# Performance work log

Measured on AMD Instinct MI355X. Metric: run time of the kernel, lower is better.

The kernel has to match this reference:

```python
import jax, jax.numpy as jnp
from jax import lax
import numpy as np

B, L, V, E = 128, 1000, 20, 32
KS = (1, 3, 5, 9, 15, 21)
NF = 20          # filters per conv branch
H_ENC = 256      # bilstm hidden per direction
H_DEC = 512
N_STEPS = 10


def conv1d(x, w, b):
    # x: [B, Cin, L], w: [Cout, Cin, K]
    p = w.shape[-1] // 2
    y = lax.conv_general_dilated(x, w, (1,), [(p, p)],
                                 dimension_numbers=('NCH', 'OIH', 'NCH'))
    return y + b[None, :, None]


def lstm_scan(seq, w_ih, w_hh, b_ih, b_hh, hidden):
    # seq: [T, B, I]; PyTorch gate order i,f,g,o
    bsz = seq.shape[1]
    h0 = jnp.zeros((bsz, hidden), seq.dtype)
    c0 = jnp.zeros((bsz, hidden), seq.dtype)
    b = b_ih + b_hh

    def step(carry, xt):
        h, c = carry
        g = xt @ w_ih.T + h @ w_hh.T + b
        i, f, gg, o = jnp.split(g, 4, axis=-1)
        c = jax.nn.sigmoid(f) * c + jax.nn.sigmoid(i) * jnp.tanh(gg)
        h = jax.nn.sigmoid(o) * jnp.tanh(c)
        return (h, c), h

    _, hs = lax.scan(step, (h0, c0), seq)
    return hs  # [T, B, hidden]


def setup_inputs() -> dict:
    key = jax.random.key(0)
    keys = iter(jax.random.split(key, 64))

    def p(shape, s=0.05):
        return jax.random.normal(next(keys), shape, jnp.float32) * s

    inp = {"x": jax.random.randint(next(keys), (B, L), 0, V)}
    inp["embed_w"] = p((V, E), 0.5).at[0].set(0.0)  # padding_idx=0
    for i, k in enumerate(KS):
        inp[f"cw{i}"] = p((NF, E, k))
        inp[f"cb{i}"] = p((NF,))
    inp["conv2_w"] = p((128, 6 * NF, 3)); inp["conv2_b"] = p((128,))
    # bilstm forward / reverse
    inp["lstm_wif"] = p((4 * H_ENC, 128)); inp["lstm_whf"] = p((4 * H_ENC, H_ENC))
    inp["lstm_bif"] = p((4 * H_ENC,));    inp["lstm_bhf"] = p((4 * H_ENC,))
    inp["lstm_wir"] = p((4 * H_ENC, 128)); inp["lstm_whr"] = p((4 * H_ENC, H_ENC))
    inp["lstm_bir"] = p((4 * H_ENC,));    inp["lstm_bhr"] = p((4 * H_ENC,))
    # decoder LSTMCell (input 1024 -> hidden 512)
    inp["dec_wi"] = p((4 * H_DEC, 2 * H_DEC)); inp["dec_wh"] = p((4 * H_DEC, H_DEC))
    inp["dec_bi"] = p((4 * H_DEC,));           inp["dec_bh"] = p((4 * H_DEC,))
    # attention + heads
    inp["attn_v"] = p((256,), 1.0)
    inp["we_w"] = p((256, 512)); inp["we_b"] = p((256,))
    inp["wd_w"] = p((256, 512)); inp["wd_b"] = p((256,))
    inp["fc_w"] = p((512, 512)); inp["fc_b"] = p((512,))
    inp["out_w"] = p((8, 512));  inp["out_b"] = p((8,))
    inp["c0"] = p((512,), 1.0)
    return inp


def reference(x, embed_w, cw0, cb0, cw1, cb1, cw2, cb2, cw3, cb3, cw4, cb4,
              cw5, cb5, conv2_w, conv2_b,
              lstm_wif, lstm_whf, lstm_bif, lstm_bhf,
              lstm_wir, lstm_whr, lstm_bir, lstm_bhr,
              dec_wi, dec_wh, dec_bi, dec_bh,
              attn_v, we_w, we_b, wd_w, wd_b, fc_w, fc_b, out_w, out_b, c0):
    bsz = x.shape[0]
    h = embed_w[x]                      # [B, L, E]
    xc = h.transpose(0, 2, 1)           # [B, E, L]
    branches = [(cw0, cb0), (cw1, cb1), (cw2, cb2), (cw3, cb3), (cw4, cb4), (cw5, cb5)]
    cnn_cat = jnp.concatenate([jax.nn.relu(conv1d(xc, w, b)) for w, b in branches], axis=1)
    feat = jax.nn.relu(conv1d(cnn_cat, conv2_w, conv2_b))  # [B, 128, L]
    seq = feat.transpose(2, 0, 1)                          # [L, B, 128]
    hs_f = lstm_scan(seq, lstm_wif, lstm_whf, lstm_bif, lstm_bhf, H_ENC)
    hs_b = lstm_scan(seq[::-1], lstm_wir, lstm_whr, lstm_bir, lstm_bhr, H_ENC)[::-1]
    lstm_out = jnp.concatenate([hs_f, hs_b], axis=-1).transpose(1, 0, 2)  # [B, L, 512]

    # encoder projection is step-invariant: precompute W_e(lstm_out)
    e_enc = jnp.einsum('blh,eh->ble', lstm_out, we_w) + we_b  # [B, L, 256]
    dec_b = dec_bi + dec_bh

    def dec_step(carry, _):
        hd, cd, ctx = carry
        inp = jnp.concatenate([ctx, hd], axis=1)             # [B, 1024]
        g = inp @ dec_wi.T + hd @ dec_wh.T + dec_b
        i, f, gg, o = jnp.split(g, 4, axis=1)
        cd = jax.nn.sigmoid(f) * cd + jax.nn.sigmoid(i) * jnp.tanh(gg)
        hd = jax.nn.sigmoid(o) * jnp.tanh(cd)
        d = hd @ wd_w.T + wd_b                               # [B, 256]
        e = jnp.tanh(e_enc + d[:, None, :])                  # [B, L, 256]
        a = e @ attn_v                                       # [B, L]
        w = jax.nn.softmax(a, axis=1)
        ctx = jnp.einsum('bl,blh->bh', w, lstm_out)          # [B, 512]
        return (hd, cd, ctx), None

    h0 = jnp.zeros((bsz, H_DEC), lstm_out.dtype)
    c0s = jnp.zeros((bsz, H_DEC), lstm_out.dtype)
    ctx0 = jnp.broadcast_to(c0, (bsz, H_DEC))
    (_, _, ctx), _ = lax.scan(dec_step, (h0, c0s, ctx0), None, length=N_STEPS)

    z = jax.nn.relu(ctx @ fc_w.T + fc_b)
    return jax.nn.sigmoid(z @ out_w.T + out_b)               # [B, 8]
```

## Files before the change

### kernel.cpp

```cpp
#include <hip/hip_runtime.h>
#include <hip/hip_bf16.h>
#include <math.h>


typedef __bf16 bf16_t;
typedef __bf16 bf16x8 __attribute__((ext_vector_type(8)));
typedef float f32x4 __attribute__((ext_vector_type(4)));

__device__ __constant__ int KBS[6]  = {1, 3, 5, 9, 15, 21};
__device__ __constant__ int WOFF[6] = {0, 1024, 4096, 9216, 18432, 33792};

__device__ inline f32x4 mfma16(bf16x8 a, bf16x8 b, f32x4 c) {
  return __builtin_amdgcn_mfma_f32_16x16x32_bf16(a, b, c, 0, 0, 0);
}
__device__ inline float sigm(float x) { return 1.f / (1.f + __expf(-x)); }
__device__ inline float tanh_fast(float x) {
  x = fminf(15.f, fmaxf(-15.f, x));
  float e = __expf(2.f * x);
  return (e - 1.f) / (e + 1.f);
}

__device__ inline void store_h_ic(bf16_t* p, bf16_t v) {
  unsigned short b = __builtin_bit_cast(unsigned short, v);
  __hip_atomic_store((unsigned short*)p, b, __ATOMIC_RELAXED, __HIP_MEMORY_SCOPE_AGENT);
}

__global__ void k_init(bf16_t* H, unsigned* bar, bf16_t* feat1p, float* cd,
                       bf16_t* dec_in, float* cbias, const float* c0,
                       const float* cb0, const float* cb1, const float* cb2,
                       const float* cb3, const float* cb4, const float* cb5) {
  int i = blockIdx.x * 256 + threadIdx.x;
  if (i < 65536) {
    unsigned* Hu = (unsigned*)H;
    size_t off = (i < 32768) ? (size_t)i : ((size_t)1001 * 32768 + (i - 32768));
    __hip_atomic_store(Hu + off, 0u, __ATOMIC_RELAXED, __HIP_MEMORY_SCOPE_AGENT);
    return;
  }
  i -= 65536;
  if (i < 512) {
    __hip_atomic_store(bar + i, 0u, __ATOMIC_RELAXED, __HIP_MEMORY_SCOPE_AGENT);
    return;
  }
  i -= 512;
  if (i < 30720) {
    int b = i / 240; int r = i - b * 240;
    int row = (r < 120) ? 0 : 1001; int c = r % 120;
    feat1p[b * 120240 + row * 120 + c] = (bf16_t)0.f; return;
  }
  i -= 30720;
  if (i < 256) { feat1p[128 * 120240 + i] = (bf16_t)0.f; return; }
  i -= 256;
  if (i < 65536) { cd[i] = 0.f; return; }
  i -= 65536;
  if (i < 131072) { int k = i & 1023; dec_in[i] = (k < 512) ? (bf16_t)c0[k] : (bf16_t)0.f; return; }
  i -= 131072;
  if (i < 120) {
    const float* cbs[6] = {cb0, cb1, cb2, cb3, cb4, cb5};
    cbias[i] = cbs[i / 20][i % 20]; return;
  }
}

__global__ void k_prep_lstm(const float* wif, const float* whf, const float* bif, const float* bhf,
                            const float* wir, const float* whr, const float* bir, const float* bhr,
                            bf16_t* Wl, float* bl) {
  int row = blockIdx.x;
  int dir = row >> 10; int np = row & 1023;
  int tile = np >> 6; int rem = np & 63; int g = rem >> 4; int u = rem & 15;
  int orow = g * 256 + tile * 16 + u;
  const float* wi = dir ? wir : wif;
  const float* wh = dir ? whr : whf;
  for (int k = threadIdx.x; k < 384; k += blockDim.x) {
    float v = (k < 128) ? wi[orow * 128 + k] : wh[orow * 256 + (k - 128)];
    Wl[row * 384 + k] = (bf16_t)v;
  }
  if (threadIdx.x == 0) {
    const float* bi = dir ? bir : bif;
    const float* bh = dir ? bhr : bhf;
    bl[row] = bi[orow] + bh[orow];
  }
}

__global__ void k_prep_dec(const float* dwi, const float* dwh, const float* dbi, const float* dbh,
                           bf16_t* Wdec, float* bdec) {
  int np = blockIdx.x;
  int tile = np >> 6; int rem = np & 63; int g = rem >> 4; int u = rem & 15;
  int orow = g * 512 + tile * 16 + u;
  for (int k = threadIdx.x; k < 1024; k += blockDim.x) {
    float v;
    if (k < 512) v = dwi[orow * 1024 + k];
    else v = dwi[orow * 1024 + 512 + (k - 512)] + dwh[orow * 512 + (k - 512)];
    Wdec[np * 1024 + k] = (bf16_t)v;
  }
  if (threadIdx.x == 0) bdec[np] = dbi[orow] + dbh[orow];
}

__global__ void k_prep_misc(const float* cw0, const float* cw1, const float* cw2,
                            const float* cw3, const float* cw4, const float* cw5,
                            const float* conv2_w, const float* we_w, const float* wd_w,
                            bf16_t* Wc1, bf16_t* Wc2, bf16_t* Wwe, bf16_t* Wwd) {
  int i = blockIdx.x * 256 + threadIdx.x;
  if (i < 55296) {
    const float* cws[6] = {cw0, cw1, cw2, cw3, cw4, cw5};
    int br = 0;
    while (br < 5 && i >= WOFF[br + 1]) ++br;
    int K = KBS[br];
    int jj = i - WOFF[br];
    int kw = K * 32;
    int f = jj / kw; int rem = jj - f * kw; int k = rem >> 5; int c = rem & 31;
    float v = (f < 20) ? cws[br][(f * 32 + c) * K + k] : 0.f;
    Wc1[i] = (bf16_t)v;
    return;
  }
  i -= 55296;
  if (i < 49152) {
    int co = i / 384; int kk = i - co * 384;
    float v = 0.f;
    if (kk < 360) { int ci = kk % 120; int k = kk / 120; v = conv2_w[co * 360 + ci * 3 + k]; }
    Wc2[i] = (bf16_t)v;
    return;
  }
  i -= 49152;
  if (i < 131072) { Wwe[i] = (bf16_t)we_w[i]; return; }
  i -= 131072;
  if (i < 131072) { Wwd[i] = (bf16_t)wd_w[i]; return; }
}

__global__ void k_embed(const int* x, const float* ew, bf16_t* embp) {
  int idx = blockIdx.x * 256 + threadIdx.x;
  if (idx >= 128 * 1020 * 32) return;
  int c = idx & 31; int rest = idx >> 5;
  int j = rest % 1020; int b = rest / 1020;
  float v = 0.f;
  int l = j - 10;
  if (l >= 0 && l < 1000) { int tok = x[b * 1000 + l]; v = ew[tok * 32 + c]; }
  embp[idx] = (bf16_t)v;
}

__global__ void __launch_bounds__(256) k_conv1(const bf16_t* __restrict__ embp,
                                               const bf16_t* __restrict__ Wc1,
                                               const float* __restrict__ cbias,
                                               bf16_t* __restrict__ feat1p) {
  int tile = blockIdx.x, br = blockIdx.y;
  int Kb = KBS[br]; int p = Kb >> 1;
  const bf16_t* Wb = Wc1 + WOFF[br];
  int tid = threadIdx.x; int w = tid >> 6; int lane = tid & 63; int u = lane & 15; int q = lane >> 4;
  const bf16_t* arow[2];
#pragma unroll
  for (int mf = 0; mf < 2; ++mf) {
    int r = tile * 128 + w * 32 + mf * 16 + u;
    int b = r / 1000, l = r - b * 1000;
    arow[mf] = embp + b * 32640 + (l + 10 - p) * 32;
  }
  f32x4 acc[2][2];
#pragma unroll
  for (int mf = 0; mf < 2; ++mf)
#pragma unroll
    for (int nf = 0; nf < 2; ++nf) acc[mf][nf] = (f32x4){0.f, 0.f, 0.f, 0.f};
  int kw = Kb * 32;
  for (int kc = 0; kc < Kb; ++kc) {
    int kk = kc * 32 + q * 8;
    bf16x8 a0 = *(const bf16x8*)(arow[0] + kk);
    bf16x8 a1 = *(const bf16x8*)(arow[1] + kk);
    bf16x8 b0 = *(const bf16x8*)(Wb + u * kw + kk);
    bf16x8 b1 = *(const bf16x8*)(Wb + (16 + u) * kw + kk);
    acc[0][0] = mfma16(a0, b0, acc[0][0]);
    acc[0][1] = mfma16(a0, b1, acc[0][1]);
    acc[1][0] = mfma16(a1, b0, acc[1][0]);
    acc[1][1] = mfma16(a1, b1, acc[1][1]);
  }
#pragma unroll
  for (int nf = 0; nf < 2; ++nf) {
    int n = nf * 16 + u;
    if (n >= 20) continue;
    int fg = br * 20 + n;
    float bias = cbias[fg];
#pragma unroll
    for (int mf = 0; mf < 2; ++mf)
#pragma unroll
      for (int reg = 0; reg < 4; ++reg) {
        int r = tile * 128 + w * 32 + mf * 16 + q * 4 + reg;
        int b = r / 1000, l = r - b * 1000;
        float v = acc[mf][nf][reg] + bias;
        v = fmaxf(v, 0.f);
        feat1p[b * 120240 + (l + 1) * 120 + fg] = (bf16_t)v;
      }
  }
}

__global__ void __launch_bounds__(256) k_conv2(const bf16_t* __restrict__ feat1p,
                                               const bf16_t* __restrict__ Wc2,
                                               const float* __restrict__ c2b,
                                               bf16_t* __restrict__ seq) {
  int tile = blockIdx.x;
  int tid = threadIdx.x; int w = tid >> 6; int lane = tid & 63; int u = lane & 15; int q = lane >> 4;
  const bf16_t* arow[2];
#pragma unroll
  for (int mf = 0; mf < 2; ++mf) {
    int r = tile * 128 + w * 32 + mf * 16 + u;
    int b = r / 1000, l = r - b * 1000;
    arow[mf] = feat1p + b * 120240 + l * 120;
  }
  f32x4 acc[2][8];
#pragma unroll
  for (int mf = 0; mf < 2; ++mf)
#pragma unroll
    for (int nf = 0; nf < 8; ++nf) acc[mf][nf] = (f32x4){0.f, 0.f, 0.f, 0.f};
#pragma unroll
  for (int kc = 0; kc < 12; ++kc) {
    int kk = kc * 32 + q * 8;
    bf16x8 a0 = *(const bf16x8*)(arow[0] + kk);
    bf16x8 a1 = *(const bf16x8*)(arow[1] + kk);
#pragma unroll
    for (int nf = 0; nf < 8; ++nf) {
      bf16x8 bfr = *(const bf16x8*)(Wc2 + (nf * 16 + u) * 384 + kk);
      acc[0][nf] = mfma16(a0, bfr, acc[0][nf]);
      acc[1][nf] = mfma16(a1, bfr, acc[1][nf]);
    }
  }
#pragma unroll
  for (int nf = 0; nf < 8; ++nf) {
    int n = nf * 16 + u;
    float bias = c2b[n];
#pragma unroll
    for (int mf = 0; mf < 2; ++mf)
#pragma unroll
      for (int reg = 0; reg < 4; ++reg) {
        int r = tile * 128 + w * 32 + mf * 16 + q * 4 + reg;
        int b = r / 1000, l = r - b * 1000;
        float v = fmaxf(acc[mf][nf][reg] + bias, 0.f);
        seq[(l * 128 + b) * 128 + n] = (bf16_t)v;
      }
  }
}

__global__ void __launch_bounds__(256) k_lstm(const bf16_t* __restrict__ seq,
                                              const bf16_t* __restrict__ Wl,
                                              const float* __restrict__ bl,
                                              bf16_t* H, unsigned* bar) {
  const int bid = blockIdx.x;
  const int dir = bid >> 4;
  const int tile = bid & 15;
  const int tid = threadIdx.x;
  const int w = tid >> 6, lane = tid & 63, u = lane & 15, q = lane >> 4;

  __shared__ __align__(16) bf16_t Wlds[64 * 392];
  const bf16_t* Wg = Wl + (size_t)(dir * 1024 + tile * 64) * 384;
  for (int i = tid; i < 64 * 48; i += 256) {
    int rr = i / 48, cc = (i - rr * 48) * 8;
    *(bf16x8*)&Wlds[rr * 392 + cc] = *(const bf16x8*)&Wg[rr * 384 + cc];
  }
  float bias[4];
#pragma unroll
  for (int g = 0; g < 4; ++g) bias[g] = bl[dir * 1024 + tile * 64 + g * 16 + u];
  __syncthreads();

  const int j = tile * 16 + u;
  const int mA0 = w * 32 + u, mA1 = w * 32 + 16 + u;
  float creg[2][4] = {{0.f, 0.f, 0.f, 0.f}, {0.f, 0.f, 0.f, 0.f}};
  unsigned* flg = bar + dir * 256;

  bf16x8 pf[2][4];
  {
    const bf16_t* seqt = seq + (size_t)(dir ? 999 : 0) * 16384;
#pragma unroll
    for (int kc = 0; kc < 4; ++kc) {
      pf[0][kc] = *(const bf16x8*)&seqt[mA0 * 128 + kc * 32 + q * 8];
      pf[1][kc] = *(const bf16x8*)&seqt[mA1 * 128 + kc * 32 + q * 8];
    }
  }

  for (int s = 0; s < 1000; ++s) {
    int t = dir ? (999 - s) : s;
    const bf16_t* hread = H + ((size_t)(dir ? (t + 2) : t) * 2 + dir) * 32768;
    bf16_t* hwrite = H + ((size_t)(t + 1) * 2 + dir) * 32768;

    bf16x8 hv0[8], hv1[8];
#pragma unroll
    for (int i = 0; i < 8; ++i) {
      hv0[i] = *(const bf16x8*)&hread[mA0 * 256 + i * 32 + q * 8];
      hv1[i] = *(const bf16x8*)&hread[mA1 * 256 + i * 32 + q * 8];
    }

    f32x4 acc[2][4];
#pragma unroll
    for (int mf = 0; mf < 2; ++mf)
#pragma unroll
      for (int g = 0; g < 4; ++g) acc[mf][g] = (f32x4){0.f, 0.f, 0.f, 0.f};

#pragma unroll
    for (int kc = 0; kc < 4; ++kc) {
      int kk = kc * 32 + q * 8;
#pragma unroll
      for (int g = 0; g < 4; ++g) {
        bf16x8 bfr = *(const bf16x8*)&Wlds[(g * 16 + u) * 392 + kk];
        acc[0][g] = mfma16(pf[0][kc], bfr, acc[0][g]);
        acc[1][g] = mfma16(pf[1][kc], bfr, acc[1][g]);
      }
    }
#pragma unroll
    for (int i = 0; i < 8; ++i) {
      int kk = 128 + i * 32 + q * 8;
#pragma unroll
      for (int g = 0; g < 4; ++g) {
        bf16x8 bfr = *(const bf16x8*)&Wlds[(g * 16 + u) * 392 + kk];
        acc[0][g] = mfma16(hv0[i], bfr, acc[0][g]);
        acc[1][g] = mfma16(hv1[i], bfr, acc[1][g]);
      }
    }

    if (s < 999) {
      const bf16_t* seqn = seq + (size_t)(dir ? (t - 1) : (t + 1)) * 16384;
#pragma unroll
      for (int kc = 0; kc < 4; ++kc) {
        pf[0][kc] = *(const bf16x8*)&seqn[mA0 * 128 + kc * 32 + q * 8];
        pf[1][kc] = *(const bf16x8*)&seqn[mA1 * 128 + kc * 32 + q * 8];
      }
    }

#pragma unroll
    for (int mf = 0; mf < 2; ++mf) {
#pragma unroll
      for (int reg = 0; reg < 4; ++reg) {
        int m = w * 32 + mf * 16 + q * 4 + reg;
        float gi = sigm(acc[mf][0][reg] + bias[0]);
        float gf = sigm(acc[mf][1][reg] + bias[1]);
        float gg = tanh_fast(acc[mf][2][reg] + bias[2]);
        float go = sigm(acc[mf][3][reg] + bias[3]);
        float c = gf * creg[mf][reg] + gi * gg;
        creg[mf][reg] = c;
        store_h_ic(&hwrite[m * 256 + j], (bf16_t)(go * tanh_fast(c)));
      }
    }

    if (s < 999) {
      __syncthreads();
      if (tid == 0)
        __hip_atomic_store(&flg[tile * 16], (unsigned)(s + 1), __ATOMIC_RELAXED,
                           __HIP_MEMORY_SCOPE_AGENT);
      if (w == 0) {
        unsigned target = (unsigned)(s + 1);
        int spins = 0;
        while (spins < (1 << 17)) {
          unsigned f = (lane < 16)
              ? __hip_atomic_load(&flg[lane * 16], __ATOMIC_RELAXED, __HIP_MEMORY_SCOPE_AGENT)
              : target;
          if (__ballot(f >= target) == ~0ull) break;
          __builtin_amdgcn_s_sleep(1);
          ++spins;
        }
      }
      __syncthreads();
    }
  }
}

__global__ void __launch_bounds__(256) k_eenc(const bf16_t* __restrict__ H,
                                              const bf16_t* __restrict__ Wwe,
                                              const float* __restrict__ we_b,
                                              bf16_t* __restrict__ e_enc) {
  int mt = blockIdx.x;
  int n0 = blockIdx.y * 64;
  int tid = threadIdx.x; int w = tid >> 6; int lane = tid & 63; int u = lane & 15; int q = lane >> 4;
  const bf16_t* af[2]; const bf16_t* ar[2];
#pragma unroll
  for (int mf = 0; mf < 2; ++mf) {
    int b = w * 32 + mf * 16 + u;
    af[mf] = H + (((size_t)(mt + 1) * 2 + 0) * 128 + b) * 256;
    ar[mf] = H + (((size_t)(mt + 1) * 2 + 1) * 128 + b) * 256;
  }
  f32x4 acc[2][4];
#pragma unroll
  for (int mf = 0; mf < 2; ++mf)
#pragma unroll
    for (int nf = 0; nf < 4; ++nf) acc[mf][nf] = (f32x4){0.f, 0.f, 0.f, 0.f};
#pragma unroll
  for (int kc = 0; kc < 16; ++kc) {
    int kk = (kc & 7) * 32 + q * 8;
    bf16x8 a0 = (kc < 8) ? *(const bf16x8*)(af[0] + kk) : *(const bf16x8*)(ar[0] + kk);
    bf16x8 a1 = (kc < 8) ? *(const bf16x8*)(af[1] + kk) : *(const bf16x8*)(ar[1] + kk);
#pragma unroll
    for (int nf = 0; nf < 4; ++nf) {
      bf16x8 bfr = *(const bf16x8*)(Wwe + (n0 + nf * 16 + u) * 512 + kc * 32 + q * 8);
      acc[0][nf] = mfma16(a0, bfr, acc[0][nf]);
      acc[1][nf] = mfma16(a1, bfr, acc[1][nf]);
    }
  }
#pragma unroll
  for (int nf = 0; nf < 4; ++nf) {
    int n = n0 + nf * 16 + u;
    float bias = we_b[n];
#pragma unroll
    for (int mf = 0; mf < 2; ++mf)
#pragma unroll
      for (int reg = 0; reg < 4; ++reg) {
        int r = mt * 128 + w * 32 + mf * 16 + q * 4 + reg;
        e_enc[(size_t)n * 128000 + r] = (bf16_t)(acc[mf][nf][reg] + bias);
      }
  }
}

__global__ void __launch_bounds__(256) k_dec_gates(const bf16_t* __restrict__ dec_in,
                                                   const bf16_t* __restrict__ Wdec,
                                                   const float* __restrict__ bdec,
                                                   float* __restrict__ cd,
                                                   bf16_t* __restrict__ hd_new) {
  int tile = blockIdx.x;
  int tid = threadIdx.x; int w = tid >> 6; int lane = tid & 63; int u = lane & 15; int q = lane >> 4;
  int j = tile * 16 + u;
  float bias[4];
#pragma unroll
  for (int g = 0; g < 4; ++g) bias[g] = bdec[tile * 64 + g * 16 + u];
  int mA0 = w * 32 + u, mA1 = w * 32 + 16 + u;
  f32x4 acc[2][4];
#pragma unroll
  for (int mf = 0; mf < 2; ++mf)
#pragma unroll
    for (int g = 0; g < 4; ++g) acc[mf][g] = (f32x4){0.f, 0.f, 0.f, 0.f};
#pragma unroll 4
  for (int kc = 0; kc < 32; ++kc) {
    int kk = kc * 32 + q * 8;
    bf16x8 a0 = *(const bf16x8*)&dec_in[mA0 * 1024 + kk];
    bf16x8 a1 = *(const bf16x8*)&dec_in[mA1 * 1024 + kk];
#pragma unroll
    for (int g = 0; g < 4; ++g) {
      bf16x8 bfr = *(const bf16x8*)&Wdec[(size_t)(tile * 64 + g * 16 + u) * 1024 + kk];
      acc[0][g] = mfma16(a0, bfr, acc[0][g]);
      acc[1][g] = mfma16(a1, bfr, acc[1][g]);
    }
  }
#pragma unroll
  for (int mf = 0; mf < 2; ++mf) {
#pragma unroll
    for (int reg = 0; reg < 4; ++reg) {
      int m = w * 32 + mf * 16 + q * 4 + reg;
      float gi = sigm(acc[mf][0][reg] + bias[0]);
      float gf = sigm(acc[mf][1][reg] + bias[1]);
      float gg = tanh_fast(acc[mf][2][reg] + bias[2]);
      float go = sigm(acc[mf][3][reg] + bias[3]);
      float c = gf * cd[m * 512 + j] + gi * gg;
      cd[m * 512 + j] = c;
      hd_new[m * 512 + j] = (bf16_t)(go * tanh_fast(c));
    }
  }
}

__global__ void __launch_bounds__(256) k_d(const bf16_t* __restrict__ hd_new,
                                           const bf16_t* __restrict__ Wwd,
                                           const float* __restrict__ wd_b,
                                           float* __restrict__ d_t) {
  int n0 = blockIdx.x * 64;
  int tid = threadIdx.x; int w = tid >> 6; int lane = tid & 63; int u = lane & 15; int q = lane >> 4;
  int mA0 = w * 32 + u, mA1 = w * 32 + 16 + u;
  f32x4 acc[2][4];
#pragma unroll
  for (int mf = 0; mf < 2; ++mf)
#pragma unroll
    for (int nf = 0; nf < 4; ++nf) acc[mf][nf] = (f32x4){0.f, 0.f, 0.f, 0.f};
#pragma unroll
  for (int kc = 0; kc < 16; ++kc) {
    int kk = kc * 32 + q * 8;
    bf16x8 a0 = *(const bf16x8*)&hd_new[mA0 * 512 + kk];
    bf16x8 a1 = *(const bf16x8*)&hd_new[mA1 * 512 + kk];
#pragma unroll
    for (int nf = 0; nf < 4; ++nf) {
      bf16x8 bfr = *(const bf16x8*)&Wwd[(n0 + nf * 16 + u) * 512 + kk];
      acc[0][nf] = mfma16(a0, bfr, acc[0][nf]);
      acc[1][nf] = mfma16(a1, bfr, acc[1][nf]);
    }
  }
#pragma unroll
  for (int nf = 0; nf < 4; ++nf) {
    int n = n0 + nf * 16 + u;
    float bias = wd_b[n];
#pragma unroll
    for (int mf = 0; mf < 2; ++mf)
#pragma unroll
      for (int reg = 0; reg < 4; ++reg) {
        int m = w * 32 + mf * 16 + q * 4 + reg;
        d_t[n * 128 + m] = acc[mf][nf][reg] + bias;
      }
  }
}

__global__ void __launch_bounds__(256) k_score(const bf16_t* __restrict__ e_enc,
                                               const float* __restrict__ d_t,
                                               const float* __restrict__ attn_v,
                                               float* __restrict__ scores) {
  int tid = threadIdx.x;
  __shared__ float vl[256];
  vl[tid] = attn_v[tid];
  __syncthreads();
  int sub = tid >> 7, b = tid & 127;
  int l = blockIdx.x * 2 + sub;
  const bf16_t* ep = e_enc + (size_t)l * 128 + b;
  const float* dp = d_t + b;
  float acc = 0.f;
#pragma unroll 8
  for (int n = 0; n < 256; ++n)
    acc += tanh_fast((float)ep[(size_t)n * 128000] + dp[n * 128]) * vl[n];
  scores[b * 1000 + l] = acc;
}

__global__ void __launch_bounds__(512) k_softmax_ctx(const float* __restrict__ scores,
                                                     const bf16_t* __restrict__ H,
                                                     const bf16_t* __restrict__ hd_new,
                                                     bf16_t* __restrict__ dec_in) {
  int b = blockIdx.x;
  int tid = threadIdx.x; int wid = tid >> 6; int lane = tid & 63;
  __shared__ float wls[1000];
  __shared__ float red[8];
  __shared__ float sh_scalar;
  float mx = -1e30f;
  for (int l = tid; l < 1000; l += 512) {
    float s = scores[b * 1000 + l];
    wls[l] = s;
    mx = fmaxf(mx, s);
  }
#pragma unroll
  for (int off = 32; off > 0; off >>= 1) mx = fmaxf(mx, __shfl_xor(mx, off));
  if (lane == 0) red[wid] = mx;
  __syncthreads();
  if (tid == 0) {
    float m2 = red[0];
#pragma unroll
    for (int i = 1; i < 8; ++i) m2 = fmaxf(m2, red[i]);
    sh_scalar = m2;
  }
  __syncthreads();
  mx = sh_scalar;
  float sum = 0.f;
  for (int l = tid; l < 1000; l += 512) {
    float p = __expf(wls[l] - mx);
    wls[l] = p;
    sum += p;
  }
#pragma unroll
  for (int off = 32; off > 0; off >>= 1) sum += __shfl_xor(sum, off);
  if (lane == 0) red[wid] = sum;
  __syncthreads();
  if (tid == 0) {
    float s2 = red[0];
#pragma unroll
    for (int i = 1; i < 8; ++i) s2 += red[i];
    sh_scalar = s2;
  }
  __syncthreads();
  float inv = 1.f / sh_scalar;
  int dirr = tid >> 8, hh = tid & 255;
  float acc = 0.f;
  const bf16_t* lp = H + (size_t)65536 + (size_t)dirr * 32768 + b * 256 + hh;
#pragma unroll 4
  for (int l = 0; l < 1000; ++l) acc += wls[l] * (float)lp[(size_t)l * 65536];
  dec_in[b * 1024 + tid] = (bf16_t)(acc * inv);
  dec_in[b * 1024 + 512 + tid] = hd_new[b * 512 + tid];
}

__global__ void __launch_bounds__(256) k_fc_out(const bf16_t* __restrict__ dec_in,
                                                const float* __restrict__ fc_w,
                                                const float* __restrict__ fc_b,
                                                const float* __restrict__ out_w,
                                                const float* __restrict__ out_b,
                                                float* __restrict__ out) {
  int b = blockIdx.x;
  int tid = threadIdx.x;
  __shared__ float ctxs[512], zs[512], parts[32][8];
  for (int jj = tid; jj < 512; jj += 256) ctxs[jj] = (float)dec_in[b * 1024 + jj];
  __syncthreads();
  for (int n = tid; n < 512; n += 256) {
    float acc = fc_b[n];
    const float* wr = fc_w + n * 512;
    for (int k = 0; k < 512; ++k) acc += ctxs[k] * wr[k];
    zs[n] = fmaxf(acc, 0.f);
  }
  __syncthreads();
  int col = tid & 7, part = tid >> 3;
  float acc = 0.f;
  const float* wo = out_w + col * 512;
  for (int k = part * 16; k < part * 16 + 16; ++k) acc += zs[k] * wo[k];
  parts[part][col] = acc;
  __syncthreads();
  if (tid < 8) {
    float a = out_b[tid];
    for (int p2 = 0; p2 < 32; ++p2) a += parts[p2][tid];
    out[b * 8 + tid] = 1.f / (1.f + __expf(-a));
  }
}

extern "C" void kernel_launch(void* const* d_in, const int* in_sizes, int n_in,
                              void* d_out, int out_size, void* d_ws, size_t ws_size,
                              hipStream_t stream) {
  const int*   x       = (const int*)d_in[0];
  const float* embed_w = (const float*)d_in[1];
  const float* cw[6]   = {(const float*)d_in[2], (const float*)d_in[4], (const float*)d_in[6],
                          (const float*)d_in[8], (const float*)d_in[10], (const float*)d_in[12]};
  const float* cb[6]   = {(const float*)d_in[3], (const float*)d_in[5], (const float*)d_in[7],
                          (const float*)d_in[9], (const float*)d_in[11], (const float*)d_in[13]};
  const float* conv2_w = (const float*)d_in[14];
  const float* conv2_b = (const float*)d_in[15];
  const float* lstm_wif = (const float*)d_in[16];
  const float* lstm_whf = (const float*)d_in[17];
  const float* lstm_bif = (const float*)d_in[18];
  const float* lstm_bhf = (const float*)d_in[19];
  const float* lstm_wir = (const float*)d_in[20];
  const float* lstm_whr = (const float*)d_in[21];
  const float* lstm_bir = (const float*)d_in[22];
  const float* lstm_bhr = (const float*)d_in[23];
  const float* dec_wi  = (const float*)d_in[24];
  const float* dec_wh  = (const float*)d_in[25];
  const float* dec_bi  = (const float*)d_in[26];
  const float* dec_bh  = (const float*)d_in[27];
  const float* attn_v  = (const float*)d_in[28];
  const float* we_w    = (const float*)d_in[29];
  const float* we_b    = (const float*)d_in[30];
  const float* wd_w    = (const float*)d_in[31];
  const float* wd_b    = (const float*)d_in[32];
  const float* fc_w    = (const float*)d_in[33];
  const float* fc_b    = (const float*)d_in[34];
  const float* out_w   = (const float*)d_in[35];
  const float* out_b   = (const float*)d_in[36];
  const float* c0      = (const float*)d_in[37];
  float* out = (float*)d_out;

  char* base = (char*)d_ws;
  bf16_t* feat1p  = (bf16_t*)(base + 0);
  bf16_t* seq     = (bf16_t*)(base + 30781952);
  bf16_t* embp    = (bf16_t*)(base + 63549952);
  bf16_t* e_enc   = (bf16_t*)(base + 0);
  char* p = base + 71905792;
  auto alloc = [&](size_t bytes) { char* r = p; p += (bytes + 255) & ~(size_t)255; return r; };
  bf16_t* H       = (bf16_t*)alloc((size_t)1002 * 65536 * 2);
  bf16_t* Wl      = (bf16_t*)alloc((size_t)2 * 1024 * 384 * 2);
  float*  bl      = (float*)alloc(2048 * 4);
  bf16_t* Wc1     = (bf16_t*)alloc(55296 * 2);
  float*  cbias   = (float*)alloc(512);
  bf16_t* Wc2     = (bf16_t*)alloc(49152 * 2);
  bf16_t* Wdec    = (bf16_t*)alloc((size_t)2048 * 1024 * 2);
  float*  bdec    = (float*)alloc(2048 * 4);
  bf16_t* Wwe     = (bf16_t*)alloc(131072 * 2);
  bf16_t* Wwd     = (bf16_t*)alloc(131072 * 2);
  unsigned* bar   = (unsigned*)alloc(512 * 4);
  bf16_t* dec_in  = (bf16_t*)alloc(131072 * 2);
  bf16_t* hd_new  = (bf16_t*)alloc(65536 * 2);
  float*  cd      = (float*)alloc(65536 * 4);
  float*  d_t     = (float*)alloc(32768 * 4);
  float*  scores  = (float*)alloc(128000 * 4);
  (void)ws_size; (void)n_in; (void)in_sizes; (void)out_size;

  k_init<<<1148, 256, 0, stream>>>(H, bar, feat1p, cd, dec_in, cbias, c0,
                                   cb[0], cb[1], cb[2], cb[3], cb[4], cb[5]);
  k_prep_lstm<<<2048, 128, 0, stream>>>(lstm_wif, lstm_whf, lstm_bif, lstm_bhf,
                                        lstm_wir, lstm_whr, lstm_bir, lstm_bhr, Wl, bl);
  k_prep_dec<<<2048, 256, 0, stream>>>(dec_wi, dec_wh, dec_bi, dec_bh, Wdec, bdec);
  k_prep_misc<<<1432, 256, 0, stream>>>(cw[0], cw[1], cw[2], cw[3], cw[4], cw[5],
                                        conv2_w, we_w, wd_w, Wc1, Wc2, Wwe, Wwd);
  k_embed<<<16320, 256, 0, stream>>>(x, embed_w, embp);
  k_conv1<<<dim3(1000, 6), 256, 0, stream>>>(embp, Wc1, cbias, feat1p);
  k_conv2<<<1000, 256, 0, stream>>>(feat1p, Wc2, conv2_b, seq);
  k_lstm<<<32, 256, 0, stream>>>(seq, Wl, bl, H, bar);
  k_eenc<<<dim3(1000, 4), 256, 0, stream>>>(H, Wwe, we_b, e_enc);
  for (int step = 0; step < 10; ++step) {
    k_dec_gates<<<32, 256, 0, stream>>>(dec_in, Wdec, bdec, cd, hd_new);
    k_d<<<4, 256, 0, stream>>>(hd_new, Wwd, wd_b, d_t);
    k_score<<<500, 256, 0, stream>>>(e_enc, d_t, attn_v, scores);
    k_softmax_ctx<<<128, 512, 0, stream>>>(scores, H, hd_new, dec_in);
  }
  k_fc_out<<<128, 256, 0, stream>>>(dec_in, fc_w, fc_b, out_w, out_b, out);
}
```

Baseline: 7.066 ms.

## Replace LSTM flag barrier with tagged h ring buffer; split context reduction

The bidirectional LSTM no longer uses a per-step flag barrier with __syncthreads and spin loops. Each h value is now written into a 4-deep ring buffer as a 32-bit word that carries the step number in its upper half. Consumers poll their own h slice until every tag matches, so each block waits only for its own data instead of on a global barrier. Separately, the attention context sum is split over 4 sequence chunks with atomicAdd into an fp32 buffer, plus a pack kernel, to raise decoder parallelism. The ring doubles the bytes per h read, and the atomics make the float sum order nondeterministic.

Result: slower. 15.02 ms (+112.6%).

```diff
diff --git a/kernel.cpp b/kernel.cpp
--- a/kernel.cpp
+++ b/kernel.cpp
@@ -6,6 +6,7 @@
 typedef __bf16 bf16_t;
 typedef __bf16 bf16x8 __attribute__((ext_vector_type(8)));
 typedef float f32x4 __attribute__((ext_vector_type(4)));
+typedef unsigned long long u64;
 
 __device__ __constant__ int KBS[6]  = {1, 3, 5, 9, 15, 21};
 __device__ __constant__ int WOFF[6] = {0, 1024, 4096, 9216, 18432, 33792};
@@ -20,28 +21,18 @@
   return (e - 1.f) / (e + 1.f);
 }
 
-__device__ inline void store_h_ic(bf16_t* p, bf16_t v) {
-  unsigned short b = __builtin_bit_cast(unsigned short, v);
-  __hip_atomic_store((unsigned short*)p, b, __ATOMIC_RELAXED, __HIP_MEMORY_SCOPE_AGENT);
-}
-
-__global__ void k_init(bf16_t* H, unsigned* bar, bf16_t* feat1p, float* cd,
-                       bf16_t* dec_in, float* cbias, const float* c0,
+__device__ inline void store_ic(unsigned* p, unsigned v) {
+  __hip_atomic_store(p, v, __ATOMIC_RELAXED, __HIP_MEMORY_SCOPE_AGENT);
+}
+__device__ inline u64 load_ic8(const u64* p) {
+  return __hip_atomic_load(p, __ATOMIC_RELAXED, __HIP_MEMORY_SCOPE_AGENT);
+}
+
+__global__ void k_init(bf16_t* feat1p, float* cd, bf16_t* dec_in, float* cbias,
+                       const float* c0,
                        const float* cb0, const float* cb1, const float* cb2,
                        const float* cb3, const float* cb4, const float* cb5) {
   int i = blockIdx.x * 256 + threadIdx.x;
-  if (i < 65536) {
-    unsigned* Hu = (unsigned*)H;
-    size_t off = (i < 32768) ? (size_t)i : ((size_t)1001 * 32768 + (i - 32768));
-    __hip_atomic_store(Hu + off, 0u, __ATOMIC_RELAXED, __HIP_MEMORY_SCOPE_AGENT);
-    return;
-  }
-  i -= 65536;
-  if (i < 512) {
-    __hip_atomic_store(bar + i, 0u, __ATOMIC_RELAXED, __HIP_MEMORY_SCOPE_AGENT);
-    return;
-  }
-  i -= 512;
   if (i < 30720) {
     int b = i / 240; int r = i - b * 240;
     int row = (r < 120) ? 0 : 1001; int c = r % 120;
@@ -233,10 +224,10 @@
   }
 }
 
-__global__ void __launch_bounds__(256) k_lstm(const bf16_t* __restrict__ seq,
-                                              const bf16_t* __restrict__ Wl,
-                                              const float* __restrict__ bl,
-                                              bf16_t* H, unsigned* bar) {
+__global__ void __launch_bounds__(256, 1) k_lstm(const bf16_t* __restrict__ seq,
+                                                 const bf16_t* __restrict__ Wl,
+                                                 const float* __restrict__ bl,
+                                                 bf16_t* H, unsigned* hx) {
   const int bid = blockIdx.x;
   const int dir = bid >> 4;
   const int tile = bid & 15;
@@ -257,7 +248,7 @@
   const int j = tile * 16 + u;
   const int mA0 = w * 32 + u, mA1 = w * 32 + 16 + u;
   float creg[2][4] = {{0.f, 0.f, 0.f, 0.f}, {0.f, 0.f, 0.f, 0.f}};
-  unsigned* flg = bar + dir * 256;
+  unsigned* ring = hx + dir * 32768;
 
   bf16x8 pf[2][4];
   {
@@ -271,14 +262,21 @@
 
   for (int s = 0; s < 1000; ++s) {
     int t = dir ? (999 - s) : s;
-    const bf16_t* hread = H + ((size_t)(dir ? (t + 2) : t) * 2 + dir) * 32768;
     bf16_t* hwrite = H + ((size_t)(t + 1) * 2 + dir) * 32768;
 
-    bf16x8 hv0[8], hv1[8];
-#pragma unroll
-    for (int i = 0; i < 8; ++i) {
-      hv0[i] = *(const bf16x8*)&hread[mA0 * 256 + i * 32 + q * 8];
-      hv1[i] = *(const bf16x8*)&hread[mA1 * 256 + i * 32 + q * 8];
+    u64 dv0[32], dv1[32];
+    const u64* a0 = nullptr; const u64* a1 = nullptr;
+    if (s > 0) {
+      const u64* rb = (const u64*)(hx + ((unsigned)(s - 1) & 3u) * 65536 + dir * 32768);
+      a0 = rb + mA0 * 128 + q * 4;
+      a1 = rb + mA1 * 128 + q * 4;
+#pragma unroll
+      for (int i = 0; i < 8; ++i)
+#pragma unroll
+        for (int pp = 0; pp < 4; ++pp) {
+          dv0[i * 4 + pp] = load_ic8(a0 + i * 16 + pp);
+          dv1[i * 4 + pp] = load_ic8(a1 + i * 16 + pp);
+        }
     }
 
     f32x4 acc[2][4];
@@ -297,14 +295,47 @@
         acc[1][g] = mfma16(pf[1][kc], bfr, acc[1][g]);
       }
     }
-#pragma unroll
-    for (int i = 0; i < 8; ++i) {
-      int kk = 128 + i * 32 + q * 8;
-#pragma unroll
-      for (int g = 0; g < 4; ++g) {
-        bf16x8 bfr = *(const bf16x8*)&Wlds[(g * 16 + u) * 392 + kk];
-        acc[0][g] = mfma16(hv0[i], bfr, acc[0][g]);
-        acc[1][g] = mfma16(hv1[i], bfr, acc[1][g]);
+
+    if (s > 0) {
+      unsigned tg = (unsigned)s;
+      int guard = 0;
+      for (;;) {
+        unsigned bad = 0;
+#pragma unroll
+        for (int i2 = 0; i2 < 32; ++i2) {
+          unsigned lo0 = (unsigned)dv0[i2], hi0 = (unsigned)(dv0[i2] >> 32);
+          unsigned lo1 = (unsigned)dv1[i2], hi1 = (unsigned)(dv1[i2] >> 32);
+          bad |= (lo0 >> 16) ^ tg;
+          bad |= (hi0 >> 16) ^ tg;
+          bad |= (lo1 >> 16) ^ tg;
+          bad |= (hi1 >> 16) ^ tg;
+        }
+        if (bad == 0 || ++guard > (1 << 17)) break;
+#pragma unroll
+        for (int i = 0; i < 8; ++i)
+#pragma unroll
+          for (int pp = 0; pp < 4; ++pp) {
+            dv0[i * 4 + pp] = load_ic8(a0 + i * 16 + pp);
+            dv1[i * 4 + pp] = load_ic8(a1 + i * 16 + pp);
+          }
+      }
+#pragma unroll
+      for (int i = 0; i < 8; ++i) {
+        union { unsigned u4[4]; bf16x8 v; } h0, h1;
+#pragma unroll
+        for (int pp = 0; pp < 4; ++pp) {
+          h0.u4[pp] = __builtin_amdgcn_perm((unsigned)(dv0[i * 4 + pp] >> 32),
+                                            (unsigned)dv0[i * 4 + pp], 0x05040100);
+          h1.u4[pp] = __builtin_amdgcn_perm((unsigned)(dv1[i * 4 + pp] >> 32),
+                                            (unsigned)dv1[i * 4 + pp], 0x05040100);
+        }
+        int kk = 128 + i * 32 + q * 8;
+#pragma unroll
+        for (int g = 0; g < 4; ++g) {
+          bf16x8 bfr = *(const bf16x8*)&Wlds[(g * 16 + u) * 392 + kk];
+          acc[0][g] = mfma16(h0.v, bfr, acc[0][g]);
+          acc[1][g] = mfma16(h1.v, bfr, acc[1][g]);
+        }
       }
     }
 
@@ -317,6 +348,8 @@
       }
     }
 
+    unsigned* rw = ring + ((unsigned)s & 3u) * 65536;
+    unsigned tagw = ((unsigned)(s + 1)) << 16;
 #pragma unroll
     for (int mf = 0; mf < 2; ++mf) {
 #pragma unroll
@@ -328,28 +361,11 @@
         float go = sigm(acc[mf][3][reg] + bias[3]);
         float c = gf * creg[mf][reg] + gi * gg;
         creg[mf][reg] = c;
-        store_h_ic(&hwrite[m * 256 + j], (bf16_t)(go * tanh_fast(c)));
-      }
-    }
-
-    if (s < 999) {
-      __syncthreads();
-      if (tid == 0)
-        __hip_atomic_store(&flg[tile * 16], (unsigned)(s + 1), __ATOMIC_RELAXED,
-                           __HIP_MEMORY_SCOPE_AGENT);
-      if (w == 0) {
-        unsigned target = (unsigned)(s + 1);
-        int spins = 0;
-        while (spins < (1 << 17)) {
-          unsigned f = (lane < 16)
-              ? __hip_atomic_load(&flg[lane * 16], __ATOMIC_RELAXED, __HIP_MEMORY_SCOPE_AGENT)
-              : target;
-          if (__ballot(f >= target) == ~0ull) break;
-          __builtin_amdgcn_s_sleep(1);
-          ++spins;
-        }
-      }
-      __syncthreads();
+        bf16_t hv = (bf16_t)(go * tanh_fast(c));
+        hwrite[m * 256 + j] = hv;
+        unsigned hb = (unsigned)__builtin_bit_cast(unsigned short, hv);
+        store_ic(&rw[m * 256 + j], tagw | hb);
+      }
     }
   }
 }
@@ -447,9 +463,12 @@
 __global__ void __launch_bounds__(256) k_d(const bf16_t* __restrict__ hd_new,
                                            const bf16_t* __restrict__ Wwd,
                                            const float* __restrict__ wd_b,
-                                           float* __restrict__ d_t) {
+                                           float* __restrict__ d_t,
+                                           float* __restrict__ ctxf) {
   int n0 = blockIdx.x * 64;
   int tid = threadIdx.x; int w = tid >> 6; int lane = tid & 63; int u = lane & 15; int q = lane >> 4;
+  int gz = blockIdx.x * 256 + tid;
+  for (int z = gz; z < 65536; z += 1024) ctxf[z] = 0.f;
   int mA0 = w * 32 + u, mA1 = w * 32 + 16 + u;
   f32x4 acc[2][4];
 #pragma unroll
@@ -501,11 +520,10 @@
   scores[b * 1000 + l] = acc;
 }
 
-__global__ void __launch_bounds__(512) k_softmax_ctx(const float* __restrict__ scores,
-                                                     const bf16_t* __restrict__ H,
-                                                     const bf16_t* __restrict__ hd_new,
-                                                     bf16_t* __restrict__ dec_in) {
-  int b = blockIdx.x;
+__global__ void __launch_bounds__(512) k_ctx(const float* __restrict__ scores,
+                                             const bf16_t* __restrict__ H,
+                                             float* __restrict__ ctxf) {
+  int chunk = blockIdx.x, b = blockIdx.y;
   int tid = threadIdx.x; int wid = tid >> 6; int lane = tid & 63;
   __shared__ float wls[1000];
   __shared__ float red[8];
@@ -548,10 +566,18 @@
   float inv = 1.f / sh_scalar;
   int dirr = tid >> 8, hh = tid & 255;
   float acc = 0.f;
-  const bf16_t* lp = H + (size_t)65536 + (size_t)dirr * 32768 + b * 256 + hh;
+  const bf16_t* lp = H + (size_t)65536 + (size_t)dirr * 32768 + b * 256 + hh +
+                     (size_t)(chunk * 250) * 65536;
 #pragma unroll 4
-  for (int l = 0; l < 1000; ++l) acc += wls[l] * (float)lp[(size_t)l * 65536];
-  dec_in[b * 1024 + tid] = (bf16_t)(acc * inv);
+  for (int l = 0; l < 250; ++l) acc += wls[chunk * 250 + l] * (float)lp[(size_t)l * 65536];
+  atomicAdd(&ctxf[b * 512 + tid], acc * inv);
+}
+
+__global__ void __launch_bounds__(512) k_pack(const float* __restrict__ ctxf,
+                                              const bf16_t* __restrict__ hd_new,
+                                              bf16_t* __restrict__ dec_in) {
+  int b = blockIdx.x; int tid = threadIdx.x;
+  dec_in[b * 1024 + tid] = (bf16_t)ctxf[b * 512 + tid];
   dec_in[b * 1024 + 512 + tid] = hd_new[b * 512 + tid];
 }
 
@@ -629,6 +655,7 @@
   char* p = base + 71905792;
   auto alloc = [&](size_t bytes) { char* r = p; p += (bytes + 255) & ~(size_t)255; return r; };
   bf16_t* H       = (bf16_t*)alloc((size_t)1002 * 65536 * 2);
+  unsigned* hx    = (unsigned*)alloc((size_t)4 * 2 * 128 * 256 * 4);
   bf16_t* Wl      = (bf16_t*)alloc((size_t)2 * 1024 * 384 * 2);
   float*  bl      = (float*)alloc(2048 * 4);
   bf16_t* Wc1     = (bf16_t*)alloc(55296 * 2);
@@ -638,16 +665,16 @@
   float*  bdec    = (float*)alloc(2048 * 4);
   bf16_t* Wwe     = (bf16_t*)alloc(131072 * 2);
   bf16_t* Wwd     = (bf16_t*)alloc(131072 * 2);
-  unsigned* bar   = (unsigned*)alloc(512 * 4);
   bf16_t* dec_in  = (bf16_t*)alloc(131072 * 2);
   bf16_t* hd_new  = (bf16_t*)alloc(65536 * 2);
   float*  cd      = (float*)alloc(65536 * 4);
   float*  d_t     = (float*)alloc(32768 * 4);
+  float*  ctxf    = (float*)alloc(65536 * 4);
   float*  scores  = (float*)alloc(128000 * 4);
   (void)ws_size; (void)n_in; (void)in_sizes; (void)out_size;
 
-  k_init<<<1148, 256, 0, stream>>>(H, bar, feat1p, cd, dec_in, cbias, c0,
-                                   cb[0], cb[1], cb[2], cb[3], cb[4], cb[5]);
+  k_init<<<890, 256, 0, stream>>>(feat1p, cd, dec_in, cbias, c0,
+                                  cb[0], cb[1], cb[2], cb[3], cb[4], cb[5]);
   k_prep_lstm<<<2048, 128, 0, stream>>>(lstm_wif, lstm_whf, lstm_bif, lstm_bhf,
                                         lstm_wir, lstm_whr, lstm_bir, lstm_bhr, Wl, bl);
   k_prep_dec<<<2048, 256, 0, stream>>>(dec_wi, dec_wh, dec_bi, dec_bh, Wdec, bdec);
@@ -656,13 +683,14 @@
   k_embed<<<16320, 256, 0, stream>>>(x, embed_w, embp);
   k_conv1<<<dim3(1000, 6), 256, 0, stream>>>(embp, Wc1, cbias, feat1p);
   k_conv2<<<1000, 256, 0, stream>>>(feat1p, Wc2, conv2_b, seq);
-  k_lstm<<<32, 256, 0, stream>>>(seq, Wl, bl, H, bar);
+  k_lstm<<<32, 256, 0, stream>>>(seq, Wl, bl, H, hx);
   k_eenc<<<dim3(1000, 4), 256, 0, stream>>>(H, Wwe, we_b, e_enc);
   for (int step = 0; step < 10; ++step) {
     k_dec_gates<<<32, 256, 0, stream>>>(dec_in, Wdec, bdec, cd, hd_new);
-    k_d<<<4, 256, 0, stream>>>(hd_new, Wwd, wd_b, d_t);
+    k_d<<<4, 256, 0, stream>>>(hd_new, Wwd, wd_b, d_t, ctxf);
     k_score<<<500, 256, 0, stream>>>(e_enc, d_t, attn_v, scores);
-    k_softmax_ctx<<<128, 512, 0, stream>>>(scores, H, hd_new, dec_in);
+    k_ctx<<<dim3(4, 128), 512, 0, stream>>>(scores, H, ctxf);
+    k_pack<<<128, 512, 0, stream>>>(ctxf, hd_new, dec_in);
   }
   k_fc_out<<<128, 256, 0, stream>>>(dec_in, fc_w, fc_b, out_w, out_b, out);
 }
```

## Use per-wave flags in LSTM recurrence and split decoder context over sequence chunks

Applied to the files above, without the earlier changes.

Replaces the block-wide __syncthreads barrier in the LSTM recurrence with per-wave flags. Each wave publishes its progress and polls only the matching waves of the other tiles. The input projection MFMAs are issued before the wait so they overlap the poll latency. It also splits the attention context reduction into four sequence chunks per batch, combined with atomicAdd into an fp32 buffer that k_d zeroes, plus a separate pack kernel. The cost is one extra launch per decoder step, non-deterministic float summation order, and subtle memory-ordering risk, since waves rely on relaxed atomics and vmcnt waits rather than block barriers.

After: 7.240 ms. 2.5% more time.

```diff
diff --git a/kernel.cpp b/kernel.cpp
--- a/kernel.cpp
+++ b/kernel.cpp
@@ -6,6 +6,7 @@
 typedef __bf16 bf16_t;
 typedef __bf16 bf16x8 __attribute__((ext_vector_type(8)));
 typedef float f32x4 __attribute__((ext_vector_type(4)));
+typedef unsigned long long u64;
 
 __device__ __constant__ int KBS[6]  = {1, 3, 5, 9, 15, 21};
 __device__ __constant__ int WOFF[6] = {0, 1024, 4096, 9216, 18432, 33792};
@@ -20,28 +21,24 @@
   return (e - 1.f) / (e + 1.f);
 }
 
+__device__ inline void store_ic(unsigned* p, unsigned v) {
+  __hip_atomic_store(p, v, __ATOMIC_RELAXED, __HIP_MEMORY_SCOPE_AGENT);
+}
+__device__ inline unsigned load_ic(const unsigned* p) {
+  return __hip_atomic_load(p, __ATOMIC_RELAXED, __HIP_MEMORY_SCOPE_AGENT);
+}
 __device__ inline void store_h_ic(bf16_t* p, bf16_t v) {
   unsigned short b = __builtin_bit_cast(unsigned short, v);
   __hip_atomic_store((unsigned short*)p, b, __ATOMIC_RELAXED, __HIP_MEMORY_SCOPE_AGENT);
 }
 
-__global__ void k_init(bf16_t* H, unsigned* bar, bf16_t* feat1p, float* cd,
-                       bf16_t* dec_in, float* cbias, const float* c0,
+__global__ void k_init(unsigned* bar, bf16_t* feat1p, float* cd, bf16_t* dec_in,
+                       float* cbias, const float* c0,
                        const float* cb0, const float* cb1, const float* cb2,
                        const float* cb3, const float* cb4, const float* cb5) {
   int i = blockIdx.x * 256 + threadIdx.x;
-  if (i < 65536) {
-    unsigned* Hu = (unsigned*)H;
-    size_t off = (i < 32768) ? (size_t)i : ((size_t)1001 * 32768 + (i - 32768));
-    __hip_atomic_store(Hu + off, 0u, __ATOMIC_RELAXED, __HIP_MEMORY_SCOPE_AGENT);
-    return;
-  }
-  i -= 65536;
-  if (i < 512) {
-    __hip_atomic_store(bar + i, 0u, __ATOMIC_RELAXED, __HIP_MEMORY_SCOPE_AGENT);
-    return;
-  }
-  i -= 512;
+  if (i < 2048) { store_ic(bar + i, 0u); return; }
+  i -= 2048;
   if (i < 30720) {
     int b = i / 240; int r = i - b * 240;
     int row = (r < 120) ? 0 : 1001; int c = r % 120;
@@ -233,10 +230,10 @@
   }
 }
 
-__global__ void __launch_bounds__(256) k_lstm(const bf16_t* __restrict__ seq,
-                                              const bf16_t* __restrict__ Wl,
-                                              const float* __restrict__ bl,
-                                              bf16_t* H, unsigned* bar) {
+__global__ void __launch_bounds__(256, 1) k_lstm(const bf16_t* __restrict__ seq,
+                                                 const bf16_t* __restrict__ Wl,
+                                                 const float* __restrict__ bl,
+                                                 bf16_t* H, unsigned* bar) {
   const int bid = blockIdx.x;
   const int dir = bid >> 4;
   const int tile = bid & 15;
@@ -257,7 +254,8 @@
   const int j = tile * 16 + u;
   const int mA0 = w * 32 + u, mA1 = w * 32 + 16 + u;
   float creg[2][4] = {{0.f, 0.f, 0.f, 0.f}, {0.f, 0.f, 0.f, 0.f}};
-  unsigned* flg = bar + dir * 256;
+  unsigned* myflag = bar + ((dir * 16 + tile) * 4 + w) * 16;
+  const unsigned* pollp = bar + ((dir * 16 + (lane & 15)) * 4 + w) * 16;
 
   bf16x8 pf[2][4];
   {
@@ -271,15 +269,12 @@
 
   for (int s = 0; s < 1000; ++s) {
     int t = dir ? (999 - s) : s;
+    bf16_t* hwrite = H + ((size_t)(t + 1) * 2 + dir) * 32768;
     const bf16_t* hread = H + ((size_t)(dir ? (t + 2) : t) * 2 + dir) * 32768;
-    bf16_t* hwrite = H + ((size_t)(t + 1) * 2 + dir) * 32768;
-
-    bf16x8 hv0[8], hv1[8];
-#pragma unroll
-    for (int i = 0; i < 8; ++i) {
-      hv0[i] = *(const bf16x8*)&hread[mA0 * 256 + i * 32 + q * 8];
-      hv1[i] = *(const bf16x8*)&hread[mA1 * 256 + i * 32 + q * 8];
-    }
+
+    unsigned tgt = (unsigned)s;
+    unsigned f0 = tgt;
+    if (s > 0 && lane < 16) f0 = load_ic(pollp);
 
     f32x4 acc[2][4];
 #pragma unroll
@@ -297,14 +292,29 @@
         acc[1][g] = mfma16(pf[1][kc], bfr, acc[1][g]);
       }
     }
-#pragma unroll
-    for (int i = 0; i < 8; ++i) {
-      int kk = 128 + i * 32 + q * 8;
-#pragma unroll
-      for (int g = 0; g < 4; ++g) {
-        bf16x8 bfr = *(const bf16x8*)&Wlds[(g * 16 + u) * 392 + kk];
-        acc[0][g] = mfma16(hv0[i], bfr, acc[0][g]);
-        acc[1][g] = mfma16(hv1[i], bfr, acc[1][g]);
+
+    if (s > 0) {
+      unsigned f = f0;
+      int guard = 0;
+      while (__ballot(f >= tgt) != ~0ull && guard < (1 << 20)) {
+        f = (lane < 16) ? load_ic(pollp) : tgt;
+        ++guard;
+      }
+      bf16x8 hv0[8], hv1[8];
+#pragma unroll
+      for (int i = 0; i < 8; ++i) {
+        hv0[i] = *(const bf16x8*)&hread[mA0 * 256 + i * 32 + q * 8];
+        hv1[i] = *(const bf16x8*)&hread[mA1 * 256 + i * 32 + q * 8];
+      }
+#pragma unroll
+      for (int i = 0; i < 8; ++i) {
+        int kk = 128 + i * 32 + q * 8;
+#pragma unroll
+        for (int g = 0; g < 4; ++g) {
+          bf16x8 bfr = *(const bf16x8*)&Wlds[(g * 16 + u) * 392 + kk];
+          acc[0][g] = mfma16(hv0[i], bfr, acc[0][g]);
+          acc[1][g] = mfma16(hv1[i], bfr, acc[1][g]);
+        }
       }
     }
 
@@ -332,25 +342,8 @@
       }
     }
 
-    if (s < 999) {
-      __syncthreads();
-      if (tid == 0)
-        __hip_atomic_store(&flg[tile * 16], (unsigned)(s + 1), __ATOMIC_RELAXED,
-                           __HIP_MEMORY_SCOPE_AGENT);
-      if (w == 0) {
-        unsigned target = (unsigned)(s + 1);
-        int spins = 0;
-        while (spins < (1 << 17)) {
-          unsigned f = (lane < 16)
-              ? __hip_atomic_load(&flg[lane * 16], __ATOMIC_RELAXED, __HIP_MEMORY_SCOPE_AGENT)
-              : target;
-          if (__ballot(f >= target) == ~0ull) break;
-          __builtin_amdgcn_s_sleep(1);
-          ++spins;
-        }
-      }
-      __syncthreads();
-    }
+    asm volatile("s_waitcnt vmcnt(0)" ::: "memory");
+    if (lane == 0) store_ic(myflag, (unsigned)(s + 1));
   }
 }
 
@@ -447,9 +440,12 @@
 __global__ void __launch_bounds__(256) k_d(const bf16_t* __restrict__ hd_new,
                                            const bf16_t* __restrict__ Wwd,
                                            const float* __restrict__ wd_b,
-                                           float* __restrict__ d_t) {
+                                           float* __restrict__ d_t,
+                                           float* __restrict__ ctxf) {
   int n0 = blockIdx.x * 64;
   int tid = threadIdx.x; int w = tid >> 6; int lane = tid & 63; int u = lane & 15; int q = lane >> 4;
+  int gz = blockIdx.x * 256 + tid;
+  for (int z = gz; z < 65536; z += 1024) ctxf[z] = 0.f;
   int mA0 = w * 32 + u, mA1 = w * 32 + 16 + u;
   f32x4 acc[2][4];
 #pragma unroll
@@ -501,11 +497,10 @@
   scores[b * 1000 + l] = acc;
 }
 
-__global__ void __launch_bounds__(512) k_softmax_ctx(const float* __restrict__ scores,
-                                                     const bf16_t* __restrict__ H,
-                                                     const bf16_t* __restrict__ hd_new,
-                                                     bf16_t* __restrict__ dec_in) {
-  int b = blockIdx.x;
+__global__ void __launch_bounds__(512) k_ctx(const float* __restrict__ scores,
+                                             const bf16_t* __restrict__ H,
+                                             float* __restrict__ ctxf) {
+  int chunk = blockIdx.x, b = blockIdx.y;
   int tid = threadIdx.x; int wid = tid >> 6; int lane = tid & 63;
   __shared__ float wls[1000];
   __shared__ float red[8];
@@ -548,10 +543,18 @@
   float inv = 1.f / sh_scalar;
   int dirr = tid >> 8, hh = tid & 255;
   float acc = 0.f;
-  const bf16_t* lp = H + (size_t)65536 + (size_t)dirr * 32768 + b * 256 + hh;
+  const bf16_t* lp = H + (size_t)65536 + (size_t)dirr * 32768 + b * 256 + hh +
+                     (size_t)(chunk * 250) * 65536;
 #pragma unroll 4
-  for (int l = 0; l < 1000; ++l) acc += wls[l] * (float)lp[(size_t)l * 65536];
-  dec_in[b * 1024 + tid] = (bf16_t)(acc * inv);
+  for (int l = 0; l < 250; ++l) acc += wls[chunk * 250 + l] * (float)lp[(size_t)l * 65536];
+  atomicAdd(&ctxf[b * 512 + tid], acc * inv);
+}
+
+__global__ void __launch_bounds__(512) k_pack(const float* __restrict__ ctxf,
+                                              const bf16_t* __restrict__ hd_new,
+                                              bf16_t* __restrict__ dec_in) {
+  int b = blockIdx.x; int tid = threadIdx.x;
+  dec_in[b * 1024 + tid] = (bf16_t)ctxf[b * 512 + tid];
   dec_in[b * 1024 + 512 + tid] = hd_new[b * 512 + tid];
 }
 
@@ -629,6 +632,7 @@
   char* p = base + 71905792;
   auto alloc = [&](size_t bytes) { char* r = p; p += (bytes + 255) & ~(size_t)255; return r; };
   bf16_t* H       = (bf16_t*)alloc((size_t)1002 * 65536 * 2);
+  unsigned* bar   = (unsigned*)alloc(2048 * 4);
   bf16_t* Wl      = (bf16_t*)alloc((size_t)2 * 1024 * 384 * 2);
   float*  bl      = (float*)alloc(2048 * 4);
   bf16_t* Wc1     = (bf16_t*)alloc(55296 * 2);
@@ -638,16 +642,16 @@
   float*  bdec    = (float*)alloc(2048 * 4);
   bf16_t* Wwe     = (bf16_t*)alloc(131072 * 2);
   bf16_t* Wwd     = (bf16_t*)alloc(131072 * 2);
-  unsigned* bar   = (unsigned*)alloc(512 * 4);
   bf16_t* dec_in  = (bf16_t*)alloc(131072 * 2);
   bf16_t* hd_new  = (bf16_t*)alloc(65536 * 2);
   float*  cd      = (float*)alloc(65536 * 4);
   float*  d_t     = (float*)alloc(32768 * 4);
+  float*  ctxf    = (float*)alloc(65536 * 4);
   float*  scores  = (float*)alloc(128000 * 4);
   (void)ws_size; (void)n_in; (void)in_sizes; (void)out_size;
 
-  k_init<<<1148, 256, 0, stream>>>(H, bar, feat1p, cd, dec_in, cbias, c0,
-                                   cb[0], cb[1], cb[2], cb[3], cb[4], cb[5]);
+  k_init<<<898, 256, 0, stream>>>(bar, feat1p, cd, dec_in, cbias, c0,
+                                  cb[0], cb[1], cb[2], cb[3], cb[4], cb[5]);
   k_prep_lstm<<<2048, 128, 0, stream>>>(lstm_wif, lstm_whf, lstm_bif, lstm_bhf,
                                         lstm_wir, lstm_whr, lstm_bir, lstm_bhr, Wl, bl);
   k_prep_dec<<<2048, 256, 0, stream>>>(dec_wi, dec_wh, dec_bi, dec_bh, Wdec, bdec);
@@ -660,9 +664,10 @@
   k_eenc<<<dim3(1000, 4), 256, 0, stream>>>(H, Wwe, we_b, e_enc);
   for (int step = 0; step < 10; ++step) {
     k_dec_gates<<<32, 256, 0, stream>>>(dec_in, Wdec, bdec, cd, hd_new);
-    k_d<<<4, 256, 0, stream>>>(hd_new, Wwd, wd_b, d_t);
+    k_d<<<4, 256, 0, stream>>>(hd_new, Wwd, wd_b, d_t, ctxf);
     k_score<<<500, 256, 0, stream>>>(e_enc, d_t, attn_v, scores);
-    k_softmax_ctx<<<128, 512, 0, stream>>>(scores, H, hd_new, dec_in);
+    k_ctx<<<dim3(4, 128), 512, 0, stream>>>(scores, H, ctxf);
+    k_pack<<<128, 512, 0, stream>>>(ctxf, hd_new, dec_in);
   }
   k_fc_out<<<128, 256, 0, stream>>>(dec_in, fc_w, fc_b, out_w, out_b, out);
 }
```
